# Kernel optimization log

Measured on AMD Instinct MI355X. Metric: run time of the kernel, lower is better.

The kernel has to match this reference:

```python
import jax, jax.numpy as jnp
import numpy as np

EPS = 1e-5
C_M = 256
C_Z = 128
C_H = 32  # hardcoded c_hidden in the module


def rms_norm(x, weight, eps=EPS):
    # x * rsqrt(mean(x^2) + eps) * weight over last axis
    ms = jnp.mean(jnp.square(x), axis=-1, keepdims=True)
    return x * jax.lax.rsqrt(ms + eps) * weight


def setup_inputs() -> dict:
    key = jax.random.key(0)
    ks = jax.random.split(key, 8)
    B, S = 256, 384
    m = jax.random.normal(ks[0], (B, S, C_M), dtype=jnp.float32)
    g_in = jnp.ones((C_M,), dtype=jnp.float32)
    Wq = jax.random.normal(ks[1], (C_M, C_H), dtype=jnp.float32) / np.sqrt(C_M)
    bq = jnp.zeros((C_H,), dtype=jnp.float32)
    Wk = jax.random.normal(ks[2], (C_M, C_H), dtype=jnp.float32) / np.sqrt(C_M)
    bk = jnp.zeros((C_H,), dtype=jnp.float32)
    # init='final' means zero-init in AF-style code, but use small random so grads flow
    Wo = jax.random.normal(ks[3], (C_H * C_H, C_Z), dtype=jnp.float32) * 0.02
    bo = jnp.zeros((C_Z,), dtype=jnp.float32)
    g_out = jnp.ones((C_Z,), dtype=jnp.float32)
    return {"m": m, "g_in": g_in, "Wq": Wq, "bq": bq, "Wk": Wk, "bk": bk,
            "Wo": Wo, "bo": bo, "g_out": g_out}


def reference(m, g_in, Wq, bq, Wk, bk, Wo, bo, g_out):
    B, S, _ = m.shape
    m_norm = rms_norm(m, g_in)                       # [B,S,c_m]
    q = m_norm @ Wq + bq                             # [B,S,c_h]
    k = m_norm @ Wk + bk                             # [B,S,c_h]
    # einsum 'bic,bjd->ijcd': sum over MSA depth b
    outer = jnp.einsum('bic,bjd->ijcd', q, k).reshape(S, S, C_H * C_H)
    z = outer @ Wo + bo                              # [S,S,c_z]
    z = rms_norm(z, g_out)
    return z.astype(jnp.float32)
```

## Files before the change

### kernel.cpp

```cpp
#include <hip/hip_runtime.h>
#include <hip/hip_bf16.h>
#include <stdint.h>

#define S   384
#define CM  256
#define CH  32
#define CZ  128
#define BB  256
#define EPS 1e-5f

typedef __attribute__((ext_vector_type(8))) short bf16x8;
typedef __attribute__((ext_vector_type(4))) float f32x4;

#define OFF_QT    0u
#define OFF_KT    6291456u
#define OFF_WT    (OFF_KT + 6291456u)
#define OFF_WOT   (OFF_WT + 32768u)

__device__ __forceinline__ unsigned short f2bf(float x) {
  union { __hip_bfloat16 h; unsigned short u; } v;
  v.h = __float2bfloat16(x);
  return v.u;
}

__device__ __forceinline__ void gload_lds16(const void* g, char* smem, uint32_t lds_off_uniform) {
  uint32_t l32 = (uint32_t)(uintptr_t)(smem + lds_off_uniform);
  __builtin_amdgcn_global_load_lds(
      (const __attribute__((address_space(1))) uint32_t*)(uintptr_t)g,
      (__attribute__((address_space(3))) uint32_t*)(uintptr_t)l32,
      16, 0, 0);
}

__device__ __forceinline__ int olds_off(int ij, int blk) {
  int slot = (blk & ~7) | (((blk & 7) ^ ((blk >> 3) & 7) ^ (ij & 7)) & 7);
  return ij * 2048 + slot * 16;
}

__global__ void k0_prep(const float* __restrict__ Wq, const float* __restrict__ Wk,
                        const float* __restrict__ Wo,
                        unsigned short* __restrict__ WTg, unsigned short* __restrict__ WoTg) {
  int idx = blockIdx.x * 256 + threadIdx.x;
  if (idx < 64 * 256) {
    int c = idx >> 8, t = idx & 255;
    float v = (c < 32) ? Wq[t * 32 + c] : Wk[t * 32 + (c - 32)];
    WTg[c * 256 + t] = f2bf(v);
  }
  int j = idx - 64 * 256;
  if (j >= 0 && j < 128 * 1024) {
    int e = j >> 10, dc = j & 1023;
    int c = dc & 31, d = dc >> 5;
    WoTg[e * 1024 + dc] = f2bf(Wo[(c * 32 + d) * 128 + e]);
  }
}

__global__ __launch_bounds__(256, 3) void k2_proj(const float* __restrict__ m,
                                                  const float* __restrict__ gin,
                                                  const unsigned short* __restrict__ WTg,
                                                  const float* __restrict__ bq,
                                                  const float* __restrict__ bk,
                                                  unsigned short* __restrict__ qT,
                                                  unsigned short* __restrict__ kT) {
  __shared__ char smem[49664] __attribute__((aligned(16)));
  const int tid = threadIdx.x;
  const int w = tid >> 6, lane = tid & 63;
  const int mlo = lane & 15, quad = lane >> 4;
  const int i0 = blockIdx.x * 4, b0 = blockIdx.y * 32;
  float* scl = (float*)(smem + 49152);

  #pragma unroll
  for (int s = 0; s < 8; ++s) {
    int C0 = (w * 8 + s) * 2;
    int c = C0 + (lane >> 5);
    int j = lane & 31;
    int t8 = (j & ~7) | ((j & 7) ^ (c & 7));
    gload_lds16(WTg + c * 256 + t8 * 8, smem, 16384u + (uint32_t)C0 * 512u);
  }

  const int rowA = tid >> 1, halfA = tid & 1;
  const int growA = (b0 + (rowA >> 2)) * S + i0 + (rowA & 3);
  {
    const float4* p = (const float4*)(m + (size_t)growA * CM + halfA * 128);
    float ss = 0.f;
    #pragma unroll 8
    for (int q4 = 0; q4 < 32; ++q4) {
      float4 x = p[q4];
      ss += x.x * x.x + x.y * x.y + x.z * x.z + x.w * x.w;
    }
    ss += __shfl_xor(ss, 1, 64);
    if (!halfA) scl[rowA] = rsqrtf(ss * (1.f / 256.f) + EPS);
  }

  f32x4 acc[2][4];
  #pragma unroll
  for (int p = 0; p < 2; ++p)
    #pragma unroll
    for (int q = 0; q < 4; ++q) acc[p][q] = (f32x4)0.f;

  for (int kb = 0; kb < 4; ++kb) {
    __syncthreads();
    {
      const int row = tid >> 1, tk0 = (tid & 1) * 32;
      const float4* pB = (const float4*)(m + (size_t)growA * CM + kb * 64 + tk0);
      const float4* pG = (const float4*)(gin + kb * 64 + tk0);
      float sc = scl[row];
      #pragma unroll
      for (int u = 0; u < 4; ++u) {
        float4 x0 = pB[u * 2], x1 = pB[u * 2 + 1];
        float4 g0 = pG[u * 2], g1 = pG[u * 2 + 1];
        union { unsigned short h[8]; int4 q; } pk;
        pk.h[0] = f2bf(x0.x * sc * g0.x); pk.h[1] = f2bf(x0.y * sc * g0.y);
        pk.h[2] = f2bf(x0.z * sc * g0.z); pk.h[3] = f2bf(x0.w * sc * g0.w);
        pk.h[4] = f2bf(x1.x * sc * g1.x); pk.h[5] = f2bf(x1.y * sc * g1.y);
        pk.h[6] = f2bf(x1.z * sc * g1.z); pk.h[7] = f2bf(x1.w * sc * g1.w);
        int blkid = (((tid & 1) * 4 + u) ^ (row & 7));
        *(int4*)(smem + row * 128 + blkid * 16) = pk.q;
      }
    }
    __syncthreads();
    #pragma unroll
    for (int ks = 0; ks < 2; ++ks) {
      bf16x8 af[2], bfr[4];
      int k8 = ks * 4 + quad;
      #pragma unroll
      for (int fm = 0; fm < 2; ++fm) {
        int mm = w * 32 + fm * 16 + mlo;
        af[fm] = *(const bf16x8*)(smem + mm * 128 + ((k8 ^ (mm & 7)) * 16));
      }
      #pragma unroll
      for (int fn = 0; fn < 4; ++fn) {
        int c = fn * 16 + mlo;
        int t8 = kb * 8 + ks * 4 + quad;
        bfr[fn] = *(const bf16x8*)(smem + 16384 + c * 512 + (((t8 & ~7) | ((t8 & 7) ^ (c & 7))) * 16));
      }
      #pragma unroll
      for (int fm = 0; fm < 2; ++fm)
        #pragma unroll
        for (int fn = 0; fn < 4; ++fn)
          acc[fm][fn] = __builtin_amdgcn_mfma_f32_16x16x32_bf16(af[fm], bfr[fn], acc[fm][fn], 0, 0, 0);
    }
  }
  __syncthreads();
  unsigned short* Cl = (unsigned short*)smem;
  #pragma unroll
  for (int fm = 0; fm < 2; ++fm)
    #pragma unroll
    for (int fn = 0; fn < 4; ++fn) {
      int cc = fn * 16 + mlo;
      float bias = (cc < 32) ? bq[cc] : bk[cc - 32];
      #pragma unroll
      for (int r = 0; r < 4; ++r) {
        int rr = w * 32 + fm * 16 + quad * 4 + r;
        Cl[rr * 72 + cc] = f2bf(acc[fm][fn][r] + bias);
      }
    }
  __syncthreads();
  {
    int il = tid >> 6, cc = tid & 63;
    unsigned short* dst = (cc < 32) ? (qT + ((i0 + il) * 32 + cc) * BB + b0)
                                    : (kT + ((i0 + il) * 32 + (cc - 32)) * BB + b0);
    #pragma unroll
    for (int v = 0; v < 4; ++v) {
      union { unsigned short h[8]; int4 q; } u;
      #pragma unroll
      for (int x = 0; x < 8; ++x) u.h[x] = Cl[((v * 8 + x) * 4 + il) * 72 + cc];
      *(int4*)(dst + v * 8) = u.q;
    }
  }
}

__global__ __launch_bounds__(512, 4) void k3_fused(const unsigned short* __restrict__ qT,
                                                   const unsigned short* __restrict__ kT,
                                                   const unsigned short* __restrict__ WoTp,
                                                   const float* __restrict__ bo,
                                                   const float* __restrict__ gout,
                                                   float* __restrict__ out) {
  __shared__ char smem[65536] __attribute__((aligned(16)));
  const int tid = threadIdx.x;
  const int w = tid >> 6, lane = tid & 63;
  const int wm = w & 3, wn = w >> 2;
  const int mlo = lane & 15, quad = lane >> 4;

  const int bid = blockIdx.x;
  const int xcd = bid & 7, idx = bid >> 3;
  const int ti = idx / 12;
  const int tj = xcd * 12 + (idx % 12);

  f32x4 acc[4][4];
  #pragma unroll
  for (int p = 0; p < 4; ++p)
    #pragma unroll
    for (int q = 0; q < 4; ++q) acc[p][q] = (f32x4)0.f;

  auto stageA = [&](int kb) {
    #pragma unroll
    for (int s = 0; s < 4; ++s) {
      int r = w * 32 + s * 8 + (lane >> 3);
      int k8 = (lane & 7) ^ (r & 7);
      gload_lds16(qT + (ti * 256 + r) * BB + kb * 64 + k8 * 8, smem, (uint32_t)(w * 32 + s * 8) * 128u);
    }
  };
  auto stageB = [&](int kb, int bsel) {
    #pragma unroll
    for (int s = 0; s < 2; ++s) {
      int r = w * 16 + s * 8 + (lane >> 3);
      int k8 = (lane & 7) ^ (r & 7);
      gload_lds16(kT + (tj * 128 + r) * BB + kb * 64 + k8 * 8, smem,
                  32768u + (uint32_t)bsel * 16384u + (uint32_t)(w * 16 + s * 8) * 128u);
    }
  };

  stageA(0); stageB(0, 0);
  __syncthreads();

  for (int kb = 0; kb < 4; ++kb) {
    const int bsel = kb & 1;
    bf16x8 afr[4], bfr[4];
    #pragma unroll
    for (int f = 0; f < 4; ++f) {
      int mm = wm * 64 + f * 16 + mlo;
      afr[f] = *(const bf16x8*)(smem + mm * 128 + ((quad ^ (mm & 7)) * 16));
    }
    #pragma unroll
    for (int f = 0; f < 4; ++f) {
      int nn = wn * 64 + f * 16 + mlo;
      bfr[f] = *(const bf16x8*)(smem + 32768 + bsel * 16384 + nn * 128 + ((quad ^ (nn & 7)) * 16));
    }
    #pragma unroll
    for (int fm = 0; fm < 4; ++fm)
      #pragma unroll
      for (int fn = 0; fn < 4; ++fn)
        acc[fm][fn] = __builtin_amdgcn_mfma_f32_16x16x32_bf16(afr[fm], bfr[fn], acc[fm][fn], 0, 0, 0);
    bf16x8 af1[4];
    #pragma unroll
    for (int f = 0; f < 4; ++f) {
      int mm = wm * 64 + f * 16 + mlo;
      af1[f] = *(const bf16x8*)(smem + mm * 128 + (((4 + quad) ^ (mm & 7)) * 16));
    }
    __syncthreads();
    if (kb < 3) { stageA(kb + 1); stageB(kb + 1, bsel ^ 1); }
    #pragma unroll
    for (int f = 0; f < 4; ++f) {
      int nn = wn * 64 + f * 16 + mlo;
      bfr[f] = *(const bf16x8*)(smem + 32768 + bsel * 16384 + nn * 128 + (((4 + quad) ^ (nn & 7)) * 16));
    }
    #pragma unroll
    for (int fm = 0; fm < 4; ++fm)
      #pragma unroll
      for (int fn = 0; fn < 4; ++fn)
        acc[fm][fn] = __builtin_amdgcn_mfma_f32_16x16x32_bf16(af1[fm], bfr[fn], acc[fm][fn], 0, 0, 0);
    __syncthreads();
  }

  #pragma unroll
  for (int fm = 0; fm < 4; ++fm)
    #pragma unroll
    for (int fn = 0; fn < 4; ++fn) {
      int col = wn * 64 + fn * 16 + mlo;
      int row0 = wm * 64 + fm * 16 + quad * 4;
      int ij = (row0 >> 5) * 4 + (col >> 5);
      int k20 = (col & 31) * 32 + (row0 & 31);
      int blk = k20 >> 3;
      int off = olds_off(ij, blk) + (k20 & 7) * 2;
      union { unsigned short h[4]; uint2 u; } pk;
      #pragma unroll
      for (int r = 0; r < 4; ++r) pk.h[r] = f2bf(acc[fm][fn][r]);
      *(uint2*)(smem + off) = pk.u;
    }
  __syncthreads();

  const int eg = w >> 1, kh = w & 1;
  const int e0 = eg * 32;
  f32x4 acc2[2][2];
  #pragma unroll
  for (int p = 0; p < 2; ++p)
    #pragma unroll
    for (int q = 0; q < 2; ++q) acc2[p][q] = (f32x4)0.f;

  #pragma unroll 4
  for (int s = 0; s < 16; ++s) {
    int kk = kh * 16 + s;
    int k = kk * 32 + quad * 8;
    int blk = kk * 4 + quad;
    bf16x8 b[2];
    #pragma unroll
    for (int fe = 0; fe < 2; ++fe)
      b[fe] = *(const bf16x8*)(WoTp + (size_t)(e0 + fe * 16 + mlo) * 1024 + k);
    #pragma unroll
    for (int fij = 0; fij < 2; ++fij) {
      int ij = fij * 16 + mlo;
      bf16x8 a = *(const bf16x8*)(smem + olds_off(ij, blk));
      #pragma unroll
      for (int fe = 0; fe < 2; ++fe)
        acc2[fij][fe] = __builtin_amdgcn_mfma_f32_16x16x32_bf16(a, b[fe], acc2[fij][fe], 0, 0, 0);
    }
  }
  __syncthreads();

  float* partf = (float*)smem;
  float* red   = (float*)(smem + 16896);
  float* sclp  = (float*)(smem + 17408);
  if (kh == 1) {
    #pragma unroll
    for (int fij = 0; fij < 2; ++fij)
      #pragma unroll
      for (int fe = 0; fe < 2; ++fe)
        #pragma unroll
        for (int r = 0; r < 4; ++r)
          partf[eg * 1056 + (fij * 16 + quad * 4 + r) * 33 + fe * 16 + mlo] = acc2[fij][fe][r];
  }
  __syncthreads();

  float v[2][2][4];
  if (kh == 0) {
    float bv[2], gv[2];
    #pragma unroll
    for (int fe = 0; fe < 2; ++fe) { bv[fe] = bo[e0 + fe * 16 + mlo]; gv[fe] = gout[e0 + fe * 16 + mlo]; }
    float sq[2][4];
    #pragma unroll
    for (int fij = 0; fij < 2; ++fij)
      #pragma unroll
      for (int r = 0; r < 4; ++r) {
        float t = 0.f;
        #pragma unroll
        for (int fe = 0; fe < 2; ++fe) {
          float x = acc2[fij][fe][r] + partf[eg * 1056 + (fij * 16 + quad * 4 + r) * 33 + fe * 16 + mlo] + bv[fe];
          v[fij][fe][r] = x * gv[fe];
          t += x * x;
        }
        sq[fij][r] = t;
      }
    #pragma unroll
    for (int o = 1; o < 16; o <<= 1)
      #pragma unroll
      for (int fij = 0; fij < 2; ++fij)
        #pragma unroll
        for (int r = 0; r < 4; ++r) sq[fij][r] += __shfl_xor(sq[fij][r], o, 64);
    if (mlo == 0) {
      #pragma unroll
      for (int fij = 0; fij < 2; ++fij)
        #pragma unroll
        for (int r = 0; r < 4; ++r) red[(fij * 16 + quad * 4 + r) * 4 + eg] = sq[fij][r];
    }
  }
  __syncthreads();
  if (tid < 32) {
    float t = red[tid * 4] + red[tid * 4 + 1] + red[tid * 4 + 2] + red[tid * 4 + 3];
    sclp[tid] = rsqrtf(t * (1.f / 128.f) + EPS);
  }
  __syncthreads();
  if (kh == 0) {
    #pragma unroll
    for (int fij = 0; fij < 2; ++fij)
      #pragma unroll
      for (int r = 0; r < 4; ++r) {
        int ij = fij * 16 + quad * 4 + r;
        float sc = sclp[ij];
        int gi = ti * 8 + (ij >> 2), gj = tj * 4 + (ij & 3);
        #pragma unroll
        for (int fe = 0; fe < 2; ++fe)
          out[((size_t)gi * S + gj) * CZ + e0 + fe * 16 + mlo] = v[fij][fe][r] * sc;
      }
  }
}

extern "C" void kernel_launch(void* const* d_in, const int* in_sizes, int n_in,
                              void* d_out, int out_size, void* d_ws, size_t ws_size,
                              hipStream_t stream) {
  const float* m    = (const float*)d_in[0];
  const float* gin  = (const float*)d_in[1];
  const float* Wq   = (const float*)d_in[2];
  const float* bq   = (const float*)d_in[3];
  const float* Wk   = (const float*)d_in[4];
  const float* bk   = (const float*)d_in[5];
  const float* Wo   = (const float*)d_in[6];
  const float* bo   = (const float*)d_in[7];
  const float* gout = (const float*)d_in[8];

  char* ws = (char*)d_ws;
  unsigned short* qT    = (unsigned short*)(ws + OFF_QT);
  unsigned short* kT    = (unsigned short*)(ws + OFF_KT);
  unsigned short* WTg   = (unsigned short*)(ws + OFF_WT);
  unsigned short* WoTp  = (unsigned short*)(ws + OFF_WOT);
  float* out = (float*)d_out;

  hipLaunchKernelGGL(k0_prep, dim3(576), dim3(256), 0, stream, Wq, Wk, Wo, WTg, WoTp);
  hipLaunchKernelGGL(k2_proj, dim3(96, 8), dim3(256), 0, stream, m, gin, WTg, bq, bk, qT, kT);
  hipLaunchKernelGGL(k3_fused, dim3(4608), dim3(512), 0, stream, qT, kT, WoTp, bo, gout, out);
}
```

Measured before the change: 390.0 us.

## Fold RMSNorm gain into weights and apply row scale after projection GEMM

The input RMSNorm gain is folded into the bf16 projection weights in the prep kernel. The per-row rsqrt scale is now applied to the GEMM accumulator instead of to each input element. The projection kernel reads m once, converting to bf16 into LDS while computing the sum of squares, which removes the second global read of m and the per-k-block syncs. The block tile drops from 32 to 16 batch rows, so the grid doubles, LDS per block grows to about 64KB and occupancy is lowered to 2 blocks per CU.

```diff
diff --git a/kernel.cpp b/kernel.cpp
--- a/kernel.cpp
+++ b/kernel.cpp
@@ -37,13 +37,13 @@
 }
 
 __global__ void k0_prep(const float* __restrict__ Wq, const float* __restrict__ Wk,
-                        const float* __restrict__ Wo,
+                        const float* __restrict__ Wo, const float* __restrict__ gin,
                         unsigned short* __restrict__ WTg, unsigned short* __restrict__ WoTg) {
   int idx = blockIdx.x * 256 + threadIdx.x;
   if (idx < 64 * 256) {
     int c = idx >> 8, t = idx & 255;
     float v = (c < 32) ? Wq[t * 32 + c] : Wk[t * 32 + (c - 32)];
-    WTg[c * 256 + t] = f2bf(v);
+    WTg[c * 256 + t] = f2bf(v * gin[t]);
   }
   int j = idx - 64 * 256;
   if (j >= 0 && j < 128 * 1024) {
@@ -53,19 +53,18 @@
   }
 }
 
-__global__ __launch_bounds__(256, 3) void k2_proj(const float* __restrict__ m,
-                                                  const float* __restrict__ gin,
+__global__ __launch_bounds__(256, 2) void k2_proj(const float* __restrict__ m,
                                                   const unsigned short* __restrict__ WTg,
                                                   const float* __restrict__ bq,
                                                   const float* __restrict__ bk,
                                                   unsigned short* __restrict__ qT,
                                                   unsigned short* __restrict__ kT) {
-  __shared__ char smem[49664] __attribute__((aligned(16)));
+  __shared__ char smem[65792] __attribute__((aligned(16)));
   const int tid = threadIdx.x;
   const int w = tid >> 6, lane = tid & 63;
   const int mlo = lane & 15, quad = lane >> 4;
-  const int i0 = blockIdx.x * 4, b0 = blockIdx.y * 32;
-  float* scl = (float*)(smem + 49152);
+  const int i0 = blockIdx.x * 4, b0 = blockIdx.y * 16;
+  float* scl = (float*)(smem + 65536);
 
   #pragma unroll
   for (int s = 0; s < 8; ++s) {
@@ -73,93 +72,74 @@
     int c = C0 + (lane >> 5);
     int j = lane & 31;
     int t8 = (j & ~7) | ((j & 7) ^ (c & 7));
-    gload_lds16(WTg + c * 256 + t8 * 8, smem, 16384u + (uint32_t)C0 * 512u);
-  }
-
-  const int rowA = tid >> 1, halfA = tid & 1;
-  const int growA = (b0 + (rowA >> 2)) * S + i0 + (rowA & 3);
+    gload_lds16(WTg + c * 256 + t8 * 8, smem, 32768u + (uint32_t)C0 * 512u);
+  }
+
   {
-    const float4* p = (const float4*)(m + (size_t)growA * CM + halfA * 128);
+    const int row = tid >> 2, part = tid & 3;
+    const size_t grow = (size_t)((b0 + (row >> 2)) * S + i0 + (row & 3)) * CM;
+    const float* pm = m + grow;
     float ss = 0.f;
-    #pragma unroll 8
-    for (int q4 = 0; q4 < 32; ++q4) {
-      float4 x = p[q4];
+    #pragma unroll
+    for (int j = 0; j < 16; ++j) {
+      int k = part * 4 + j * 16;
+      float4 x = *(const float4*)(pm + k);
       ss += x.x * x.x + x.y * x.y + x.z * x.z + x.w * x.w;
+      union { unsigned short h[4]; uint2 q; } pk;
+      pk.h[0] = f2bf(x.x); pk.h[1] = f2bf(x.y); pk.h[2] = f2bf(x.z); pk.h[3] = f2bf(x.w);
+      int blk = (k >> 3) ^ (row & 7);
+      *(uint2*)(smem + row * 512 + blk * 16 + (k & 7) * 2) = pk.q;
     }
     ss += __shfl_xor(ss, 1, 64);
-    if (!halfA) scl[rowA] = rsqrtf(ss * (1.f / 256.f) + EPS);
-  }
-
-  f32x4 acc[2][4];
-  #pragma unroll
-  for (int p = 0; p < 2; ++p)
-    #pragma unroll
-    for (int q = 0; q < 4; ++q) acc[p][q] = (f32x4)0.f;
-
+    ss += __shfl_xor(ss, 2, 64);
+    if (part == 0) scl[row] = rsqrtf(ss * (1.f / 256.f) + EPS);
+  }
+  __syncthreads();
+
+  f32x4 acc[4];
+  #pragma unroll
+  for (int q = 0; q < 4; ++q) acc[q] = (f32x4)0.f;
+  #pragma unroll
   for (int kb = 0; kb < 4; ++kb) {
-    __syncthreads();
-    {
-      const int row = tid >> 1, tk0 = (tid & 1) * 32;
-      const float4* pB = (const float4*)(m + (size_t)growA * CM + kb * 64 + tk0);
-      const float4* pG = (const float4*)(gin + kb * 64 + tk0);
-      float sc = scl[row];
-      #pragma unroll
-      for (int u = 0; u < 4; ++u) {
-        float4 x0 = pB[u * 2], x1 = pB[u * 2 + 1];
-        float4 g0 = pG[u * 2], g1 = pG[u * 2 + 1];
-        union { unsigned short h[8]; int4 q; } pk;
-        pk.h[0] = f2bf(x0.x * sc * g0.x); pk.h[1] = f2bf(x0.y * sc * g0.y);
-        pk.h[2] = f2bf(x0.z * sc * g0.z); pk.h[3] = f2bf(x0.w * sc * g0.w);
-        pk.h[4] = f2bf(x1.x * sc * g1.x); pk.h[5] = f2bf(x1.y * sc * g1.y);
-        pk.h[6] = f2bf(x1.z * sc * g1.z); pk.h[7] = f2bf(x1.w * sc * g1.w);
-        int blkid = (((tid & 1) * 4 + u) ^ (row & 7));
-        *(int4*)(smem + row * 128 + blkid * 16) = pk.q;
-      }
-    }
-    __syncthreads();
     #pragma unroll
     for (int ks = 0; ks < 2; ++ks) {
-      bf16x8 af[2], bfr[4];
       int k8 = ks * 4 + quad;
-      #pragma unroll
-      for (int fm = 0; fm < 2; ++fm) {
-        int mm = w * 32 + fm * 16 + mlo;
-        af[fm] = *(const bf16x8*)(smem + mm * 128 + ((k8 ^ (mm & 7)) * 16));
-      }
+      int mm = w * 16 + mlo;
+      bf16x8 af = *(const bf16x8*)(smem + mm * 512 + kb * 128 + ((k8 ^ (mm & 7)) * 16));
       #pragma unroll
       for (int fn = 0; fn < 4; ++fn) {
         int c = fn * 16 + mlo;
-        int t8 = kb * 8 + ks * 4 + quad;
-        bfr[fn] = *(const bf16x8*)(smem + 16384 + c * 512 + (((t8 & ~7) | ((t8 & 7) ^ (c & 7))) * 16));
+        int t8 = kb * 8 + k8;
+        bf16x8 bfr = *(const bf16x8*)(smem + 32768 + c * 512 + (((t8 & ~7) | ((t8 & 7) ^ (c & 7))) * 16));
+        acc[fn] = __builtin_amdgcn_mfma_f32_16x16x32_bf16(af, bfr, acc[fn], 0, 0, 0);
       }
-      #pragma unroll
-      for (int fm = 0; fm < 2; ++fm)
-        #pragma unroll
-        for (int fn = 0; fn < 4; ++fn)
-          acc[fm][fn] = __builtin_amdgcn_mfma_f32_16x16x32_bf16(af[fm], bfr[fn], acc[fm][fn], 0, 0, 0);
-    }
-  }
-  __syncthreads();
+    }
+  }
+  __syncthreads();
+
   unsigned short* Cl = (unsigned short*)smem;
-  #pragma unroll
-  for (int fm = 0; fm < 2; ++fm)
+  {
+    float sr[4];
+    #pragma unroll
+    for (int r = 0; r < 4; ++r) sr[r] = scl[w * 16 + quad * 4 + r];
     #pragma unroll
     for (int fn = 0; fn < 4; ++fn) {
       int cc = fn * 16 + mlo;
       float bias = (cc < 32) ? bq[cc] : bk[cc - 32];
       #pragma unroll
       for (int r = 0; r < 4; ++r) {
-        int rr = w * 32 + fm * 16 + quad * 4 + r;
-        Cl[rr * 72 + cc] = f2bf(acc[fm][fn][r] + bias);
+        int rr = w * 16 + quad * 4 + r;
+        Cl[rr * 72 + cc] = f2bf(acc[fn][r] * sr[r] + bias);
       }
     }
+  }
   __syncthreads();
   {
     int il = tid >> 6, cc = tid & 63;
     unsigned short* dst = (cc < 32) ? (qT + ((i0 + il) * 32 + cc) * BB + b0)
                                     : (kT + ((i0 + il) * 32 + (cc - 32)) * BB + b0);
     #pragma unroll
-    for (int v = 0; v < 4; ++v) {
+    for (int v = 0; v < 2; ++v) {
       union { unsigned short h[8]; int4 q; } u;
       #pragma unroll
       for (int x = 0; x < 8; ++x) u.h[x] = Cl[((v * 8 + x) * 4 + il) * 72 + cc];
@@ -383,7 +363,7 @@
   unsigned short* WoTp  = (unsigned short*)(ws + OFF_WOT);
   float* out = (float*)d_out;
 
-  hipLaunchKernelGGL(k0_prep, dim3(576), dim3(256), 0, stream, Wq, Wk, Wo, WTg, WoTp);
-  hipLaunchKernelGGL(k2_proj, dim3(96, 8), dim3(256), 0, stream, m, gin, WTg, bq, bk, qT, kT);
+  hipLaunchKernelGGL(k0_prep, dim3(576), dim3(256), 0, stream, Wq, Wk, Wo, gin, WTg, WoTp);
+  hipLaunchKernelGGL(k2_proj, dim3(96, 16), dim3(256), 0, stream, m, WTg, bq, bk, qT, kT);
   hipLaunchKernelGGL(k3_fused, dim3(4608), dim3(512), 0, stream, qT, kT, WoTp, bo, gout, out);
 }
```

Measured after the change: 393.5 us. Within noise of the previous version (+0.9%).
